# Optimization experiments

Hardware: AMD Instinct MI355X
Metric: run time of the kernel (lower is better)

## Reference

```python
import jax, jax.numpy as jnp
import numpy as np

B, T, D = 4, 2048, 1024
H = 16
DH = D // H
BASE = 10000.0


def _rope_tables(seq_len, dim):
    inv_freq = 1.0 / (BASE ** (np.arange(0, dim, 2, dtype=np.float32) / dim))
    pos = np.arange(seq_len, dtype=np.float32)
    freqs = np.outer(pos, inv_freq)            # (T, dim/2)
    emb = np.concatenate([freqs, freqs], -1)   # (T, dim)
    return jnp.asarray(np.cos(emb)), jnp.asarray(np.sin(emb))


def setup_inputs() -> dict:
    key = jax.random.key(0)
    ks = jax.random.split(key, 5)
    s = 1.0 / np.sqrt(D)
    x = jax.random.normal(ks[0], (B, T, D), jnp.float32)
    Wqkv = jax.random.normal(ks[1], (D, 3 * D), jnp.float32) * s
    bqkv = jnp.zeros((3 * D,), jnp.float32)
    Wproj = jax.random.normal(ks[2], (D, D), jnp.float32) * s
    bproj = jnp.zeros((D,), jnp.float32)
    cos, sin = _rope_tables(T, DH)
    return {"x": x, "Wqkv": Wqkv, "bqkv": bqkv, "Wproj": Wproj,
            "bproj": bproj, "cos": cos, "sin": sin}


def _rotate_half(u):
    u1, u2 = jnp.split(u, 2, axis=-1)
    return jnp.concatenate([-u2, u1], axis=-1)


def reference(x, Wqkv, bqkv, Wproj, bproj, cos, sin):
    b, t, d = x.shape
    qkv = x @ Wqkv + bqkv                       # (B, T, 3D)
    qkv = qkv.reshape(b, t, 3, H, DH)           # matches '(three h d)' order
    q, k, v = qkv[:, :, 0], qkv[:, :, 1], qkv[:, :, 2]  # (B, T, H, DH)
    c = cos[None, :, None, :]                   # (1, T, 1, DH)
    s = sin[None, :, None, :]
    q = q * c + _rotate_half(q) * s
    k = k * c + _rotate_half(k) * s
    scale = DH ** -0.5
    attn = jnp.einsum('bthd,bshd->bhts', q, k) * scale   # (B, H, T, T)
    attn = jax.nn.softmax(attn, axis=-1)
    out = jnp.einsum('bhts,bshd->bthd', attn, v)          # (B, T, H, DH)
    out = out.reshape(b, t, d)
    return out @ Wproj + bproj
```

## Files before the change

### kernel.cpp

```cpp
#include <hip/hip_runtime.h>


typedef _Float16 half_t;
typedef _Float16 half8 __attribute__((ext_vector_type(8)));
typedef _Float16 half4v __attribute__((ext_vector_type(4)));
typedef float floatx4 __attribute__((ext_vector_type(4)));

#define MFMA_F16 __builtin_amdgcn_mfma_f32_16x16x32_f16

constexpr int Bdim = 4, T = 2048, D = 1024, H = 16, DH = 64;
constexpr int Mrows = Bdim * T;
constexpr int N1 = 3 * D;
constexpr int KD = D;

constexpr float QSCALE = 0.125f * 1.4426950408889634f;
constexpr float CSHIFT = 4.0f * 1.4426950408889634f;

__device__ __forceinline__ void gl_lds16(const half_t* g, half_t* l) {
  __builtin_amdgcn_global_load_lds(
      (const __attribute__((address_space(1))) void*)g,
      (__attribute__((address_space(3))) void*)l, 16, 0, 0);
}

__global__ __launch_bounds__(256) void cvt_kernel(const float* __restrict__ s,
                                                  half_t* __restrict__ d, int n4) {
  int i = blockIdx.x * 256 + threadIdx.x;
  if (i < n4) {
    float4 v = ((const float4*)s)[i];
    half4v h;
    h[0] = (half_t)v.x; h[1] = (half_t)v.y; h[2] = (half_t)v.z; h[3] = (half_t)v.w;
    ((half4v*)d)[i] = h;
  }
}

__global__ __launch_bounds__(64) void cvt_transpose(const float* __restrict__ W,
                                                    half_t* __restrict__ Wt,
                                                    int Kr, int Nc) {
  __shared__ half_t Th[32][36];
  const int l = threadIdx.x;
  const int n0 = blockIdx.x * 32, k0 = blockIdx.y * 32;
#pragma unroll
  for (int i = 0; i < 4; ++i) {
    int kk = (l >> 3) + i * 8;
    int nn4 = (l & 7) * 4;
    float4 v = *(const float4*)(W + (size_t)(k0 + kk) * Nc + n0 + nn4);
    half4v h;
    h[0] = (half_t)v.x; h[1] = (half_t)v.y; h[2] = (half_t)v.z; h[3] = (half_t)v.w;
    *(half4v*)&Th[kk][nn4] = h;
  }
  __syncthreads();
#pragma unroll
  for (int i = 0; i < 4; ++i) {
    int nn = (l >> 3) + i * 8;
    int kk4 = (l & 7) * 4;
    half4v h;
#pragma unroll
    for (int j = 0; j < 4; ++j) h[j] = Th[kk4 + j][nn];
    *(half4v*)(Wt + (size_t)(n0 + nn) * Kr + k0 + kk4) = h;
  }
}

__global__ __launch_bounds__(256) void gemm_qkv_rope(
    const half_t* __restrict__ X, const half_t* __restrict__ Wt,
    const float* __restrict__ bias, const float* __restrict__ cosT,
    const float* __restrict__ sinT,
    half_t* __restrict__ Q, half_t* __restrict__ K, half_t* __restrict__ V) {
  __shared__ half_t As[128 * 32];
  __shared__ half_t Bs[128 * 32];
  const int tid = threadIdx.x;
  const int lane = tid & 63, wv = tid >> 6;
  const int wm = wv >> 1, wn = wv & 1;
  const int qd = lane >> 4, ln = lane & 15;
  const int bn = blockIdx.x, bm = blockIdx.y;

  floatx4 acc[4][4] = {};

  for (int k0 = 0; k0 < KD; k0 += 32) {
#pragma unroll
    for (int p = 0; p < 2; ++p) {
      int c = tid + p * 256;
      int row = c >> 2, col = (c & 3) << 3;
      gl_lds16(X + (size_t)(bm * 128 + row) * KD + k0 + col, As + c * 8);
      gl_lds16(Wt + (size_t)(bn * 128 + row) * KD + k0 + col, Bs + c * 8);
    }
    __syncthreads();

    half8 af[4], bf[4];
#pragma unroll
    for (int mi = 0; mi < 4; ++mi)
      af[mi] = *(const half8*)&As[(wm * 64 + mi * 16 + ln) * 32 + qd * 8];
#pragma unroll
    for (int ni = 0; ni < 4; ++ni)
      bf[ni] = *(const half8*)&Bs[(wn * 64 + ni * 16 + ln) * 32 + qd * 8];
#pragma unroll
    for (int mi = 0; mi < 4; ++mi)
#pragma unroll
      for (int ni = 0; ni < 4; ++ni)
        acc[mi][ni] = MFMA_F16(af[mi], bf[ni], acc[mi][ni], 0, 0, 0);
    __syncthreads();
  }

  const int n0 = bn * 128 + wn * 64;
  const int sreg = n0 >> 10;
  const int h = (n0 & 1023) >> 6;
  float bv[4];
#pragma unroll
  for (int ni = 0; ni < 4; ++ni) bv[ni] = bias[n0 + ni * 16 + ln];

  if (sreg == 2) {
#pragma unroll
    for (int mi = 0; mi < 4; ++mi) {
      int m0 = bm * 128 + wm * 64 + mi * 16 + qd * 4;
      int b = m0 >> 11, t0 = m0 & (T - 1);
#pragma unroll
      for (int ni = 0; ni < 4; ++ni) {
        int dh = ni * 16 + ln;
        half4v hv;
#pragma unroll
        for (int r = 0; r < 4; ++r) hv[r] = (half_t)(acc[mi][ni][r] + bv[ni]);
        *(half4v*)(V + ((size_t)(b * H + h) * DH + dh) * T + t0) = hv;
      }
    }
  } else {
    const float qscale = (sreg == 0) ? QSCALE : 1.0f;
    half_t* OUT = (sreg == 0) ? Q : K;
#pragma unroll
    for (int mi = 0; mi < 4; ++mi) {
#pragma unroll
      for (int r = 0; r < 4; ++r) {
        int m = bm * 128 + wm * 64 + mi * 16 + qd * 4 + r;
        int b = m >> 11, t = m & (T - 1);
        float v0 = acc[mi][0][r] + bv[0];
        float v1 = acc[mi][1][r] + bv[1];
        float v2 = acc[mi][2][r] + bv[2];
        float v3 = acc[mi][3][r] + bv[3];
        float c0 = cosT[t * 64 + ln],      s0 = sinT[t * 64 + ln];
        float c1 = cosT[t * 64 + 16 + ln], s1 = sinT[t * 64 + 16 + ln];
        float c2 = cosT[t * 64 + 32 + ln], s2 = sinT[t * 64 + 32 + ln];
        float c3 = cosT[t * 64 + 48 + ln], s3 = sinT[t * 64 + 48 + ln];
        float o0 = v0 * c0 - v2 * s0;
        float o1 = v1 * c1 - v3 * s1;
        float o2 = v2 * c2 + v0 * s2;
        float o3 = v3 * c3 + v1 * s3;
        size_t base = ((size_t)(b * H + h) * T + t) * DH;
        OUT[base + 0 * 16 + ln] = (half_t)(o0 * qscale);
        OUT[base + 1 * 16 + ln] = (half_t)(o1 * qscale);
        OUT[base + 2 * 16 + ln] = (half_t)(o2 * qscale);
        OUT[base + 3 * 16 + ln] = (half_t)(o3 * qscale);
      }
    }
  }
}

__global__ __launch_bounds__(512, 4) void flash_attn(
    const half_t* __restrict__ Q, const half_t* __restrict__ K,
    const half_t* __restrict__ Vt, half_t* __restrict__ AO) {
  __shared__ __align__(16) half_t Klds[64 * 64];
  __shared__ __align__(16) half_t Vlds[64 * 64];
  __shared__ __align__(16) half_t Pw[8][32 * 64];
  const int tid = threadIdx.x;
  const int lane = tid & 63, wv = tid >> 6;
  const int qd = lane >> 4, ln = lane & 15;
  const int bh = blockIdx.y;
  const int q0 = blockIdx.x * 256 + wv * 32;
  const half_t* Qb = Q + (size_t)bh * T * DH;
  const half_t* Kb = K + (size_t)bh * T * DH;
  const half_t* Vb = Vt + (size_t)bh * DH * T;
  half_t* Pq = Pw[wv];
  const int swz = (ln & 7) << 3;

  const int sr = tid >> 3, sc8 = (tid & 7) << 3;
  const int stoff = sr * 64 + (sc8 ^ ((sr & 7) << 3));
  const half_t* Kg = Kb + (size_t)sr * DH + sc8;
  const half_t* Vg = Vb + (size_t)sr * T + sc8;

  half8 qf[2][2];
#pragma unroll
  for (int mi = 0; mi < 2; ++mi)
#pragma unroll
    for (int ks = 0; ks < 2; ++ks)
      qf[mi][ks] = *(const half8*)(Qb + (size_t)(q0 + mi * 16 + ln) * DH + ks * 32 + qd * 8);

  floatx4 Oacc[2][4] = {};
  float Ls[2] = {0.f, 0.f};

  half8 kreg = *(const half8*)Kg;
  half8 vreg = *(const half8*)Vg;

  for (int s0 = 0; s0 < T; s0 += 64) {
    *(half8*)&Klds[stoff] = kreg;
    *(half8*)&Vlds[stoff] = vreg;
    __syncthreads();

    if (s0 + 64 < T) {
      kreg = *(const half8*)(Kg + (size_t)(s0 + 64) * DH);
      vreg = *(const half8*)(Vg + (s0 + 64));
    }

#pragma unroll
    for (int ni = 0; ni < 4; ++ni) {
      floatx4 s4[2] = {};
#pragma unroll
      for (int ks = 0; ks < 2; ++ks) {
        int krow = ni * 16 + ln;
        half8 kf = *(const half8*)&Klds[krow * 64 + (((ks * 32) | (qd * 8)) ^ swz)];
        __builtin_amdgcn_s_setprio(1);
#pragma unroll
        for (int mi = 0; mi < 2; ++mi)
          s4[mi] = MFMA_F16(kf, qf[mi][ks], s4[mi], 0, 0, 0);
        __builtin_amdgcn_s_setprio(0);
      }
#pragma unroll
      for (int mi = 0; mi < 2; ++mi) {
        float p0 = __builtin_amdgcn_exp2f(s4[mi][0] - CSHIFT);
        float p1 = __builtin_amdgcn_exp2f(s4[mi][1] - CSHIFT);
        float p2 = __builtin_amdgcn_exp2f(s4[mi][2] - CSHIFT);
        float p3 = __builtin_amdgcn_exp2f(s4[mi][3] - CSHIFT);
        Ls[mi] += (p0 + p1) + (p2 + p3);
        half4v h; h[0] = (half_t)p0; h[1] = (half_t)p1; h[2] = (half_t)p2; h[3] = (half_t)p3;
        int row = mi * 16 + ln;
        int chunk = ni * 16 + ((qd >> 1) << 3);
        int low = (qd & 1) << 2;
        *(half4v*)&Pq[row * 64 + (chunk ^ swz) + low] = h;
      }
    }

#pragma unroll
    for (int ks = 0; ks < 2; ++ks) {
      half8 pf[2];
#pragma unroll
      for (int mi = 0; mi < 2; ++mi)
        pf[mi] = *(const half8*)&Pq[(mi * 16 + ln) * 64 + (((ks * 32) | (qd * 8)) ^ swz)];
#pragma unroll
      for (int di = 0; di < 4; ++di) {
        half8 vf = *(const half8*)&Vlds[(di * 16 + ln) * 64 + (((ks * 32) | (qd * 8)) ^ swz)];
        __builtin_amdgcn_s_setprio(1);
#pragma unroll
        for (int mi = 0; mi < 2; ++mi)
          Oacc[mi][di] = MFMA_F16(pf[mi], vf, Oacc[mi][di], 0, 0, 0);
        __builtin_amdgcn_s_setprio(0);
      }
    }
    __syncthreads();
  }

#pragma unroll
  for (int mi = 0; mi < 2; ++mi) {
    Ls[mi] += __shfl_xor(Ls[mi], 16);
    Ls[mi] += __shfl_xor(Ls[mi], 32);
  }

  const int b = bh >> 4, h = bh & 15;
#pragma unroll
  for (int mi = 0; mi < 2; ++mi) {
#pragma unroll
    for (int r = 0; r < 4; ++r) {
      float invL = 1.f / __shfl(Ls[mi], qd * 4 + r);
      int t = q0 + mi * 16 + qd * 4 + r;
      size_t base = ((size_t)b * T + t) * D + h * DH;
#pragma unroll
      for (int di = 0; di < 4; ++di)
        AO[base + di * 16 + ln] = (half_t)(Oacc[mi][di][r] * invL);
    }
  }
}

__global__ __launch_bounds__(256) void gemm_proj(
    const half_t* __restrict__ X, const half_t* __restrict__ Wt,
    const float* __restrict__ bias, float* __restrict__ OUTF) {
  __shared__ half_t As[128 * 32];
  __shared__ half_t Bs[128 * 32];
  const int tid = threadIdx.x;
  const int lane = tid & 63, wv = tid >> 6;
  const int wm = wv >> 1, wn = wv & 1;
  const int qd = lane >> 4, ln = lane & 15;
  const int bn = blockIdx.x, bm = blockIdx.y;

  floatx4 acc[4][4] = {};

  for (int k0 = 0; k0 < KD; k0 += 32) {
#pragma unroll
    for (int p = 0; p < 2; ++p) {
      int c = tid + p * 256;
      int row = c >> 2, col = (c & 3) << 3;
      gl_lds16(X + (size_t)(bm * 128 + row) * KD + k0 + col, As + c * 8);
      gl_lds16(Wt + (size_t)(bn * 128 + row) * KD + k0 + col, Bs + c * 8);
    }
    __syncthreads();

    half8 af[4], bf[4];
#pragma unroll
    for (int mi = 0; mi < 4; ++mi)
      af[mi] = *(const half8*)&As[(wm * 64 + mi * 16 + ln) * 32 + qd * 8];
#pragma unroll
    for (int ni = 0; ni < 4; ++ni)
      bf[ni] = *(const half8*)&Bs[(wn * 64 + ni * 16 + ln) * 32 + qd * 8];
#pragma unroll
    for (int mi = 0; mi < 4; ++mi)
#pragma unroll
      for (int ni = 0; ni < 4; ++ni)
        acc[mi][ni] = MFMA_F16(af[mi], bf[ni], acc[mi][ni], 0, 0, 0);
    __syncthreads();
  }

  const int n0 = bn * 128 + wn * 64;
  float bv[4];
#pragma unroll
  for (int ni = 0; ni < 4; ++ni) bv[ni] = bias[n0 + ni * 16 + ln];
#pragma unroll
  for (int mi = 0; mi < 4; ++mi) {
#pragma unroll
    for (int r = 0; r < 4; ++r) {
      int m = bm * 128 + wm * 64 + mi * 16 + qd * 4 + r;
#pragma unroll
      for (int ni = 0; ni < 4; ++ni)
        OUTF[(size_t)m * D + n0 + ni * 16 + ln] = acc[mi][ni][r] + bv[ni];
    }
  }
}

extern "C" void kernel_launch(void* const* d_in, const int* in_sizes, int n_in,
                              void* d_out, int out_size, void* d_ws, size_t ws_size,
                              hipStream_t stream) {
  const float* x     = (const float*)d_in[0];
  const float* Wqkv  = (const float*)d_in[1];
  const float* bqkv  = (const float*)d_in[2];
  const float* Wproj = (const float*)d_in[3];
  const float* bproj = (const float*)d_in[4];
  const float* cosT  = (const float*)d_in[5];
  const float* sinT  = (const float*)d_in[6];
  float* out = (float*)d_out;

  half_t* xh      = (half_t*)d_ws;
  half_t* Wqkvt   = xh + (size_t)Mrows * KD;
  half_t* Wprojt  = Wqkvt + (size_t)KD * N1;
  half_t* Qb      = Wprojt + (size_t)D * D;
  half_t* Kb      = Qb + (size_t)Bdim * H * T * DH;
  half_t* Vb      = Kb + (size_t)Bdim * H * T * DH;
  half_t* AO      = xh;

  cvt_kernel<<<(Mrows * KD / 4 + 255) / 256, 256, 0, stream>>>(x, xh, Mrows * KD / 4);
  cvt_transpose<<<dim3(N1 / 32, KD / 32), 64, 0, stream>>>(Wqkv, Wqkvt, KD, N1);
  cvt_transpose<<<dim3(D / 32, KD / 32), 64, 0, stream>>>(Wproj, Wprojt, KD, D);

  gemm_qkv_rope<<<dim3(N1 / 128, Mrows / 128), 256, 0, stream>>>(
      xh, Wqkvt, bqkv, cosT, sinT, Qb, Kb, Vb);
  flash_attn<<<dim3(T / 256, Bdim * H), 512, 0, stream>>>(Qb, Kb, Vb, AO);
  gemm_proj<<<dim3(D / 128, Mrows / 128), 256, 0, stream>>>(AO, Wprojt, bproj, out);
}
```

Baseline: 289.0 us.

## Triple-buffer GEMM K-loop with async LDS prefetch and swizzle block order

```diff
diff --git a/kernel.cpp b/kernel.cpp
--- a/kernel.cpp
+++ b/kernel.cpp
@@ -12,6 +12,7 @@
 constexpr int Mrows = Bdim * T;
 constexpr int N1 = 3 * D;
 constexpr int KD = D;
+constexpr int NT = KD / 32;
 
 constexpr float QSCALE = 0.125f * 1.4426950408889634f;
 constexpr float CSHIFT = 4.0f * 1.4426950408889634f;
@@ -60,44 +61,72 @@
   }
 }
 
-__global__ __launch_bounds__(256) void gemm_qkv_rope(
+__global__ __launch_bounds__(256, 3) void gemm_qkv_rope(
     const half_t* __restrict__ X, const half_t* __restrict__ Wt,
     const float* __restrict__ bias, const float* __restrict__ cosT,
     const float* __restrict__ sinT,
     half_t* __restrict__ Q, half_t* __restrict__ K, half_t* __restrict__ V) {
-  __shared__ half_t As[128 * 32];
-  __shared__ half_t Bs[128 * 32];
+  __shared__ half_t As[3 * 128 * 32];
+  __shared__ half_t Bs[3 * 128 * 32];
   const int tid = threadIdx.x;
   const int lane = tid & 63, wv = tid >> 6;
   const int wm = wv >> 1, wn = wv & 1;
   const int qd = lane >> 4, ln = lane & 15;
-  const int bn = blockIdx.x, bm = blockIdx.y;
+  const int flat = blockIdx.y * 24 + blockIdx.x;
+  const int swzb = (flat & 7) * 192 + (flat >> 3);
+  const int bn = swzb % 24, bm = swzb / 24;
+
+  const int srow = tid >> 2, scol = (tid & 3) << 3;
+  const half_t* Xg = X + (size_t)(bm * 128 + srow) * KD + scol;
+  const half_t* Wg = Wt + (size_t)(bn * 128 + srow) * KD + scol;
 
   floatx4 acc[4][4] = {};
 
-  for (int k0 = 0; k0 < KD; k0 += 32) {
+#pragma unroll
+  for (int pt = 0; pt < 2; ++pt) {
 #pragma unroll
     for (int p = 0; p < 2; ++p) {
       int c = tid + p * 256;
       int row = c >> 2, col = (c & 3) << 3;
-      gl_lds16(X + (size_t)(bm * 128 + row) * KD + k0 + col, As + c * 8);
-      gl_lds16(Wt + (size_t)(bn * 128 + row) * KD + k0 + col, Bs + c * 8);
-    }
-    __syncthreads();
-
+      gl_lds16(X + (size_t)(bm * 128 + row) * KD + pt * 32 + col, As + pt * 4096 + c * 8);
+      gl_lds16(Wt + (size_t)(bn * 128 + row) * KD + pt * 32 + col, Bs + pt * 4096 + c * 8);
+    }
+  }
+  asm volatile("s_waitcnt vmcnt(4)" ::: "memory");
+  __builtin_amdgcn_s_barrier();
+
+  int rd = 0, st = 2;
+  for (int t = 0; t < NT; ++t) {
+    if (t + 2 < NT) {
+#pragma unroll
+      for (int p = 0; p < 2; ++p) {
+        int c = tid + p * 256;
+        int row = c >> 2, col = (c & 3) << 3;
+        gl_lds16(X + (size_t)(bm * 128 + row) * KD + (t + 2) * 32 + col, As + st * 4096 + c * 8);
+        gl_lds16(Wt + (size_t)(bn * 128 + row) * KD + (t + 2) * 32 + col, Bs + st * 4096 + c * 8);
+      }
+    }
+    const half_t* Ab = As + rd * 4096;
+    const half_t* Bb = Bs + rd * 4096;
     half8 af[4], bf[4];
 #pragma unroll
     for (int mi = 0; mi < 4; ++mi)
-      af[mi] = *(const half8*)&As[(wm * 64 + mi * 16 + ln) * 32 + qd * 8];
+      af[mi] = *(const half8*)&Ab[(wm * 64 + mi * 16 + ln) * 32 + qd * 8];
 #pragma unroll
     for (int ni = 0; ni < 4; ++ni)
-      bf[ni] = *(const half8*)&Bs[(wn * 64 + ni * 16 + ln) * 32 + qd * 8];
+      bf[ni] = *(const half8*)&Bb[(wn * 64 + ni * 16 + ln) * 32 + qd * 8];
+    __builtin_amdgcn_s_setprio(1);
 #pragma unroll
     for (int mi = 0; mi < 4; ++mi)
 #pragma unroll
       for (int ni = 0; ni < 4; ++ni)
         acc[mi][ni] = MFMA_F16(af[mi], bf[ni], acc[mi][ni], 0, 0, 0);
-    __syncthreads();
+    __builtin_amdgcn_s_setprio(0);
+    if (t + 2 < NT) asm volatile("s_waitcnt vmcnt(4)" ::: "memory");
+    else            asm volatile("s_waitcnt vmcnt(0)" ::: "memory");
+    __builtin_amdgcn_s_barrier();
+    rd = (rd == 2) ? 0 : rd + 1;
+    st = (st == 2) ? 0 : st + 1;
   }
 
   const int n0 = bn * 128 + wn * 64;
@@ -161,8 +190,10 @@
   const int tid = threadIdx.x;
   const int lane = tid & 63, wv = tid >> 6;
   const int qd = lane >> 4, ln = lane & 15;
-  const int bh = blockIdx.y;
-  const int q0 = blockIdx.x * 256 + wv * 32;
+  const int flat = blockIdx.y * 8 + blockIdx.x;
+  const int swzb = (flat & 7) * 64 + (flat >> 3);
+  const int bh = swzb >> 3;
+  const int q0 = (swzb & 7) * 256 + wv * 32;
   const half_t* Qb = Q + (size_t)bh * T * DH;
   const half_t* Kb = K + (size_t)bh * T * DH;
   const half_t* Vb = Vt + (size_t)bh * DH * T;
@@ -265,42 +296,66 @@
   }
 }
 
-__global__ __launch_bounds__(256) void gemm_proj(
+__global__ __launch_bounds__(256, 3) void gemm_proj(
     const half_t* __restrict__ X, const half_t* __restrict__ Wt,
     const float* __restrict__ bias, float* __restrict__ OUTF) {
-  __shared__ half_t As[128 * 32];
-  __shared__ half_t Bs[128 * 32];
+  __shared__ half_t As[3 * 128 * 32];
+  __shared__ half_t Bs[3 * 128 * 32];
   const int tid = threadIdx.x;
   const int lane = tid & 63, wv = tid >> 6;
   const int wm = wv >> 1, wn = wv & 1;
   const int qd = lane >> 4, ln = lane & 15;
-  const int bn = blockIdx.x, bm = blockIdx.y;
+  const int flat = blockIdx.y * 8 + blockIdx.x;
+  const int swzb = (flat & 7) * 64 + (flat >> 3);
+  const int bn = swzb % 8, bm = swzb / 8;
 
   floatx4 acc[4][4] = {};
 
-  for (int k0 = 0; k0 < KD; k0 += 32) {
+#pragma unroll
+  for (int pt = 0; pt < 2; ++pt) {
 #pragma unroll
     for (int p = 0; p < 2; ++p) {
       int c = tid + p * 256;
       int row = c >> 2, col = (c & 3) << 3;
-      gl_lds16(X + (size_t)(bm * 128 + row) * KD + k0 + col, As + c * 8);
-      gl_lds16(Wt + (size_t)(bn * 128 + row) * KD + k0 + col, Bs + c * 8);
-    }
-    __syncthreads();
-
+      gl_lds16(X + (size_t)(bm * 128 + row) * KD + pt * 32 + col, As + pt * 4096 + c * 8);
+      gl_lds16(Wt + (size_t)(bn * 128 + row) * KD + pt * 32 + col, Bs + pt * 4096 + c * 8);
+    }
+  }
+  asm volatile("s_waitcnt vmcnt(4)" ::: "memory");
+  __builtin_amdgcn_s_barrier();
+
+  int rd = 0, st = 2;
+  for (int t = 0; t < NT; ++t) {
+    if (t + 2 < NT) {
+#pragma unroll
+      for (int p = 0; p < 2; ++p) {
+        int c = tid + p * 256;
+        int row = c >> 2, col = (c & 3) << 3;
+        gl_lds16(X + (size_t)(bm * 128 + row) * KD + (t + 2) * 32 + col, As + st * 4096 + c * 8);
+        gl_lds16(Wt + (size_t)(bn * 128 + row) * KD + (t + 2) * 32 + col, Bs + st * 4096 + c * 8);
+      }
+    }
+    const half_t* Ab = As + rd * 4096;
+    const half_t* Bb = Bs + rd * 4096;
     half8 af[4], bf[4];
 #pragma unroll
     for (int mi = 0; mi < 4; ++mi)
-      af[mi] = *(const half8*)&As[(wm * 64 + mi * 16 + ln) * 32 + qd * 8];
+      af[mi] = *(const half8*)&Ab[(wm * 64 + mi * 16 + ln) * 32 + qd * 8];
 #pragma unroll
     for (int ni = 0; ni < 4; ++ni)
-      bf[ni] = *(const half8*)&Bs[(wn * 64 + ni * 16 + ln) * 32 + qd * 8];
+      bf[ni] = *(const half8*)&Bb[(wn * 64 + ni * 16 + ln) * 32 + qd * 8];
+    __builtin_amdgcn_s_setprio(1);
 #pragma unroll
     for (int mi = 0; mi < 4; ++mi)
 #pragma unroll
       for (int ni = 0; ni < 4; ++ni)
         acc[mi][ni] = MFMA_F16(af[mi], bf[ni], acc[mi][ni], 0, 0, 0);
-    __syncthreads();
+    __builtin_amdgcn_s_setprio(0);
+    if (t + 2 < NT) asm volatile("s_waitcnt vmcnt(4)" ::: "memory");
+    else            asm volatile("s_waitcnt vmcnt(0)" ::: "memory");
+    __builtin_amdgcn_s_barrier();
+    rd = (rd == 2) ? 0 : rd + 1;
+    st = (st == 2) ? 0 : st + 1;
   }
 
   const int n0 = bn * 128 + wn * 64;
```

After: 289.9 us. Within noise of the previous version (+0.3%).
